# Optimization experiments

Hardware: AMD Instinct MI355X
Metric: run time of the kernel (lower is better)

## Reference

```python
import jax, jax.numpy as jnp
import numpy as np

BATCH, SEQ, N_INPUT, N_HIDDEN, N_OUTPUT = 256, 512, 512, 128, 2


def setup_inputs() -> dict:
    key = jax.random.key(0)
    ks = jax.random.split(key, 6)
    s_i = 1.0 / np.sqrt(N_INPUT)
    s_h = 1.0 / np.sqrt(N_HIDDEN)
    return {
        "x": jax.random.normal(ks[0], (BATCH, SEQ, N_INPUT), dtype=jnp.float32),
        # LSTM gate kernels, gate order (i, f, g, o) concatenated on last axis.
        # flax nn.LSTMCell: dense_i has no bias, dense_h has bias.
        "Wi": jax.random.normal(ks[1], (N_INPUT, 4 * N_HIDDEN), dtype=jnp.float32) * s_i,
        "Wh": jax.random.normal(ks[2], (N_HIDDEN, 4 * N_HIDDEN), dtype=jnp.float32) * s_h,
        "b": jax.random.normal(ks[3], (4 * N_HIDDEN,), dtype=jnp.float32) * 0.01,
        "Wd": jax.random.normal(ks[4], (N_HIDDEN, N_OUTPUT), dtype=jnp.float32) * s_h,
        "bd": jax.random.normal(ks[5], (N_OUTPUT,), dtype=jnp.float32) * 0.01,
    }


def reference(x, Wi, Wh, b, Wd, bd):
    B, S, _ = x.shape
    H = Wh.shape[0]
    # Precompute input projection for all steps in one big GEMM: (S, B, 4H)
    x_gates = jnp.einsum('bsi,ig->sbg', x, Wi)

    def step(carry, xg):
        c, h = carry
        gates = xg + h @ Wh + b  # (B, 4H)
        i, f, g, o = jnp.split(gates, 4, axis=-1)
        c = jax.nn.sigmoid(f) * c + jax.nn.sigmoid(i) * jnp.tanh(g)
        h = jax.nn.sigmoid(o) * jnp.tanh(c)
        return (c, h), h

    c0 = jnp.zeros((B, H), dtype=x.dtype)
    h0 = jnp.zeros((B, H), dtype=x.dtype)
    (_, h_last), _ = jax.lax.scan(step, (c0, h0), x_gates)
    logits = h_last @ Wd + bd  # (B, N_OUTPUT)
    return logits
```

## Files before the change

kernel.cpp:

```cpp
#include <hip/hip_runtime.h>
#include <hip/hip_bf16.h>


typedef __attribute__((ext_vector_type(8))) short short8;
typedef __attribute__((ext_vector_type(4))) float floatx4;
typedef __attribute__((ext_vector_type(4))) unsigned short ushortx4;
typedef __attribute__((ext_vector_type(2))) unsigned int uint2v;

#define LOG2E 1.44269504088896340736f

__device__ __forceinline__ unsigned short f2bf(float f) {
  unsigned int u = __builtin_bit_cast(unsigned int, f);
  u = (u + 0x7fffu + ((u >> 16) & 1u)) >> 16;
  return (unsigned short)u;
}
__device__ __forceinline__ float bf2f(unsigned short u) {
  unsigned int v = ((unsigned int)u) << 16;
  return __builtin_bit_cast(float, v);
}
__device__ __forceinline__ float sigf(float x) {
  return __builtin_amdgcn_rcpf(1.0f + __builtin_amdgcn_exp2f(-LOG2E * x));
}
__device__ __forceinline__ float tanhf_(float x) {
  return 1.0f - 2.0f * __builtin_amdgcn_rcpf(1.0f + __builtin_amdgcn_exp2f(2.0f * LOG2E * x));
}
__device__ __forceinline__ void bar_lds() {
  asm volatile("s_waitcnt lgkmcnt(0)" ::: "memory");
  __builtin_amdgcn_s_barrier();
  __builtin_amdgcn_sched_barrier(0);
}
__device__ __forceinline__ void gl_lds16(const void* g, void* l) {
  __builtin_amdgcn_global_load_lds(
      (const __attribute__((address_space(1))) unsigned int*)g,
      (__attribute__((address_space(3))) unsigned int*)l, 16, 0, 0);
}

__global__ void pack_kernel(const float* __restrict__ Wi, const float* __restrict__ Wh,
                            unsigned short* __restrict__ Wi_p, unsigned short* __restrict__ Wh_p,
                            unsigned int* __restrict__ flags) {
  if (blockIdx.x == 0 && threadIdx.x < 8) flags[threadIdx.x] = 0u;
  int idx = blockIdx.x * 256 + threadIdx.x;
  if (idx < 262144) {
    int j = idx & 7, lane = (idx >> 3) & 63, nt = (idx >> 9) & 31, kk = idx >> 14;
    int k = kk * 32 + ((lane >> 4) * 8) + j;
    int n = nt * 16 + (lane & 15);
    Wi_p[idx] = f2bf(Wi[k * 512 + n]);
  } else {
    int i2 = idx - 262144;
    int j = i2 & 7, lane = (i2 >> 3) & 63, nt = (i2 >> 9) & 31, kk = i2 >> 14;
    int k = kk * 32 + ((lane >> 4) * 8) + j;
    int n = nt * 16 + (lane & 15);
    Wh_p[i2] = f2bf(Wh[k * 512 + n]);
  }
}

__global__ __launch_bounds__(512, 2) void fused_kernel(
    const float* __restrict__ x, const unsigned short* __restrict__ Wi_p,
    const float* __restrict__ bias, unsigned int* __restrict__ xg5,
    const unsigned short* __restrict__ Wh_p, const float* __restrict__ Wd,
    const float* __restrict__ bd, float* __restrict__ out,
    unsigned int* __restrict__ flags) {
  __shared__ __align__(16) unsigned short As[128 * 72];
  __shared__ __align__(16) unsigned short Bs[2 * 32 * 64 * 8];
  __shared__ __align__(16) unsigned short hb[2 * 16 * 140];
  __shared__ __align__(16) float gbw[8 * 320];

  const int tid = threadIdx.x;
  const int lane = tid & 63;
  const int w = tid >> 6;
  const int quad = lane >> 4;
  const int lm = lane & 15;

  if (blockIdx.x < 192) {
    const int wm = w >> 2, wn = w & 3;

    float bs_[4][2];
    #pragma unroll
    for (int g = 0; g < 4; ++g)
      #pragma unroll
      for (int jc = 0; jc < 2; ++jc)
        bs_[g][jc] = bias[g * 128 + wn * 32 + jc * 16 + lm];

    for (int t = blockIdx.x; t < 1024; t += 192) {
      const int s = t >> 1;
      const int b0 = (t & 1) * 128;

      floatx4 acc[4][8];
      #pragma unroll
      for (int a = 0; a < 4; ++a)
        #pragma unroll
        for (int b2 = 0; b2 < 8; ++b2) { acc[a][b2].x = 0.f; acc[a][b2].y = 0.f; acc[a][b2].z = 0.f; acc[a][b2].w = 0.f; }

      const float* xbase = x + ((size_t)(b0 + w * 16 + quad) * 512 + s) * 512 + lm * 4;

      floatx4 cur[4], nxt[4];
      #pragma unroll
      for (int i = 0; i < 4; ++i)
        cur[i] = *(const floatx4*)(xbase + (size_t)i * 1048576);

      for (int kt = 0; kt < 8; ++kt) {
        bar_lds();
        #pragma unroll
        for (int i = 0; i < 4; ++i) {
          int r = w * 16 + i * 4 + quad;
          ushortx4 u;
          u.x = f2bf(cur[i].x); u.y = f2bf(cur[i].y); u.z = f2bf(cur[i].z); u.w = f2bf(cur[i].w);
          *(ushortx4*)(&As[r * 72 + lm * 4]) = u;
        }
        #pragma unroll
        for (int c = 0; c < 8; ++c) {
          int kg = c & 1, ntl = (c >> 1) * 8 + w;
          const unsigned short* src = Wi_p + ((size_t)((kt * 2 + kg) * 32 + ntl) * 64 + lane) * 8;
          unsigned short* dst = &Bs[(size_t)((kg * 32 + ntl) * 64) * 8];
          gl_lds16(src, dst);
        }
        __builtin_amdgcn_sched_barrier(0);
        if (kt < 7) {
          #pragma unroll
          for (int i = 0; i < 4; ++i)
            nxt[i] = *(const floatx4*)(xbase + (size_t)i * 1048576 + (kt + 1) * 64);
          asm volatile("s_waitcnt vmcnt(4) lgkmcnt(0)" ::: "memory");
        } else {
          asm volatile("s_waitcnt vmcnt(0) lgkmcnt(0)" ::: "memory");
        }
        __builtin_amdgcn_s_barrier();
        __builtin_amdgcn_sched_barrier(0);
        #pragma unroll
        for (int ks = 0; ks < 2; ++ks) {
          short8 af[4];
          #pragma unroll
          for (int mt = 0; mt < 4; ++mt) {
            int m = wm * 64 + mt * 16 + lm;
            af[mt] = *(const short8*)(&As[m * 72 + ks * 32 + quad * 8]);
          }
          #pragma unroll
          for (int nt = 0; nt < 8; ++nt) {
            int g = nt >> 1, jc = nt & 1;
            int ntl = g * 8 + wn * 2 + jc;
            short8 bfv = *(const short8*)(&Bs[(size_t)((ks * 32 + ntl) * 64 + lane) * 8]);
            #pragma unroll
            for (int mt = 0; mt < 4; ++mt)
              acc[mt][nt] = __builtin_amdgcn_mfma_f32_16x16x32_bf16(af[mt], bfv, acc[mt][nt], 0, 0, 0);
          }
        }
        #pragma unroll
        for (int i = 0; i < 4; ++i) cur[i] = nxt[i];
      }
      #pragma unroll
      for (int mt = 0; mt < 4; ++mt) {
        int bbase = b0 + wm * 64 + mt * 16 + quad * 4;
        #pragma unroll
        for (int jc = 0; jc < 2; ++jc) {
          int wv = wn * 2 + jc;
          #pragma unroll
          for (int rr = 0; rr < 4; ++rr) {
            size_t cell = ((size_t)s * 64 + ((bbase + rr) >> 2)) * 512 + wv * 64 + rr * 16 + lm;
            float g0 = acc[mt][0 + jc][rr] + bs_[0][jc];
            float g1 = acc[mt][2 + jc][rr] + bs_[1][jc];
            float g2 = acc[mt][4 + jc][rr] + bs_[2][jc];
            float g3 = acc[mt][6 + jc][rr] + bs_[3][jc];
            uint2v v;
            v.x = (unsigned int)f2bf(g0) | ((unsigned int)f2bf(g1) << 16);
            v.y = (unsigned int)f2bf(g2) | ((unsigned int)f2bf(g3) << 16);
            *(uint2v*)(xg5 + cell * 2) = v;
          }
        }
      }
      __syncthreads();
      if (tid == 0)
        __hip_atomic_fetch_add(&flags[t >> 7], 1u, __ATOMIC_RELEASE, __HIP_MEMORY_SCOPE_AGENT);
    }
  } else {
    const int bb = blockIdx.x - 192;

    for (int i = tid; i < 2 * 16 * 140; i += 512) hb[i] = 0;

    short8 bfr[4][4];
    #pragma unroll
    for (int kk = 0; kk < 4; ++kk)
      #pragma unroll
      for (int g = 0; g < 4; ++g)
        bfr[kk][g] = *(const short8*)(Wh_p + ((size_t)(kk * 32 + g * 8 + w) * 64 + lane) * 8);

    float cst = 0.f;

    const unsigned int* xp = xg5 + ((size_t)bb * 512 + tid) * 2;
    float* gw = gbw + w * 320;

    while (__hip_atomic_load(&flags[0], __ATOMIC_ACQUIRE, __HIP_MEMORY_SCOPE_AGENT) < 128u)
      __builtin_amdgcn_s_sleep(2);

    uint2v xga = *(const uint2v*)(xp);
    uint2v xgb = *(const uint2v*)(xp + 65536);

    __syncthreads();

    auto substep = [&](const int rp, uint2v& xcur, int spre) {
      uint2v xv = xcur;
      if (spre < 512)
        xcur = *(const uint2v*)(xp + (size_t)spre * 65536);

      short8 af[4];
      #pragma unroll
      for (int kk = 0; kk < 4; ++kk) {
        const unsigned short* p = &hb[rp * 2240 + lm * 140 + kk * 32 + quad * 8];
        union { short8 v; ushortx4 h[2]; } t;
        t.h[0] = *(const ushortx4*)(p);
        t.h[1] = *(const ushortx4*)(p + 4);
        af[kk] = t.v;
      }
      floatx4 acc[4];
      #pragma unroll
      for (int g = 0; g < 4; ++g) { acc[g].x = 0.f; acc[g].y = 0.f; acc[g].z = 0.f; acc[g].w = 0.f; }
      #pragma unroll
      for (int kk = 0; kk < 4; ++kk)
        #pragma unroll
        for (int g = 0; g < 4; ++g)
          acc[g] = __builtin_amdgcn_mfma_f32_16x16x32_bf16(af[kk], bfr[kk][g], acc[g], 0, 0, 0);

      if (lane < 16) {
        #pragma unroll
        for (int r = 0; r < 4; ++r) {
          floatx4 t4;
          t4.x = acc[0][r]; t4.y = acc[1][r]; t4.z = acc[2][r]; t4.w = acc[3][r];
          *(floatx4*)(gw + lm * 20 + r * 4) = t4;
        }
      }
      asm volatile("s_waitcnt lgkmcnt(0)" ::: "memory");
      __builtin_amdgcn_sched_barrier(0);
      floatx4 gv = *(const floatx4*)(gw + lm * 20 + quad * 4);

      float pre0 = gv.x + bf2f((unsigned short)(xv.x & 0xffffu));
      float pre1 = gv.y + bf2f((unsigned short)(xv.x >> 16));
      float pre2 = gv.z + bf2f((unsigned short)(xv.y & 0xffffu));
      float pre3 = gv.w + bf2f((unsigned short)(xv.y >> 16));
      float cc = sigf(pre1) * cst + sigf(pre0) * tanhf_(pre2);
      cst = cc;
      float hv = sigf(pre3) * tanhf_(cc);
      hb[(rp ^ 1) * 2240 + quad * 140 + w * 16 + lm] = f2bf(hv);
      bar_lds();
    };

    for (int c = 0; c < 8; ++c) {
      if (c < 7) {
        while (__hip_atomic_load(&flags[c + 1], __ATOMIC_ACQUIRE, __HIP_MEMORY_SCOPE_AGENT) < 128u)
          __builtin_amdgcn_s_sleep(2);
      }
      #pragma unroll 1
      for (int s2 = 0; s2 < 64; s2 += 2) {
        int s = c * 64 + s2;
        substep(0, xga, s + 2);
        substep(1, xgb, s + 3);
      }
    }

    if (tid < 8) {
      int rw = tid >> 1, co = tid & 1;
      float a = bd[co];
      for (int j2 = 0; j2 < 128; ++j2)
        a += bf2f(hb[rw * 140 + j2]) * Wd[j2 * 2 + co];
      out[(bb * 4 + rw) * 2 + co] = a;
    }
  }
}

extern "C" void kernel_launch(void* const* d_in, const int* in_sizes, int n_in,
                              void* d_out, int out_size, void* d_ws, size_t ws_size,
                              hipStream_t stream) {
  const float* x  = (const float*)d_in[0];
  const float* Wi = (const float*)d_in[1];
  const float* Wh = (const float*)d_in[2];
  const float* b  = (const float*)d_in[3];
  const float* Wd = (const float*)d_in[4];
  const float* bd = (const float*)d_in[5];
  float* out = (float*)d_out;

  unsigned short* Wi_p = (unsigned short*)d_ws;
  unsigned short* Wh_p = Wi_p + 262144;
  unsigned int*   flags = (unsigned int*)(Wh_p + 65536);
  unsigned int*   xg5  = flags + 128;

  pack_kernel<<<1280, 256, 0, stream>>>(Wi, Wh, Wi_p, Wh_p, flags);
  fused_kernel<<<256, 512, 0, stream>>>(x, Wi_p, b, xg5, Wh_p, Wd, bd, out, flags);
}
```

Baseline: 798.8 us.

## Use relaxed atomic xgate transfers and single-wave chunk flag polling

The producer blocks now write the bf16 gate pre-activations with 64-bit relaxed agent-scope atomic stores. The recurrent blocks read them with matching atomic loads. Only wave 0 of each recurrent block spins on the chunk flag, and it polls the current chunk rather than the next one; the other waves then pass an LDS barrier and reload the first two steps' inputs at each chunk start. This is meant to cut polling traffic and keep cross-block data coherent, but it drops the one-chunk lookahead and uses relaxed ordering in place of acquire, so the consumer may stall at chunk boundaries and could read stale data.

```diff
diff --git a/kernel.cpp b/kernel.cpp
--- a/kernel.cpp
+++ b/kernel.cpp
@@ -159,14 +159,16 @@
             float g1 = acc[mt][2 + jc][rr] + bs_[1][jc];
             float g2 = acc[mt][4 + jc][rr] + bs_[2][jc];
             float g3 = acc[mt][6 + jc][rr] + bs_[3][jc];
-            uint2v v;
-            v.x = (unsigned int)f2bf(g0) | ((unsigned int)f2bf(g1) << 16);
-            v.y = (unsigned int)f2bf(g2) | ((unsigned int)f2bf(g3) << 16);
-            *(uint2v*)(xg5 + cell * 2) = v;
+            unsigned long long v64 =
+                (unsigned long long)((unsigned int)f2bf(g0) | ((unsigned int)f2bf(g1) << 16)) |
+                ((unsigned long long)((unsigned int)f2bf(g2) | ((unsigned int)f2bf(g3) << 16)) << 32);
+            __hip_atomic_store((unsigned long long*)xg5 + cell, v64,
+                               __ATOMIC_RELAXED, __HIP_MEMORY_SCOPE_AGENT);
           }
         }
       }
       __syncthreads();
+      __builtin_amdgcn_sched_barrier(0);
       if (tid == 0)
         __hip_atomic_fetch_add(&flags[t >> 7], 1u, __ATOMIC_RELEASE, __HIP_MEMORY_SCOPE_AGENT);
     }
@@ -184,21 +186,22 @@
 
     float cst = 0.f;
 
-    const unsigned int* xp = xg5 + ((size_t)bb * 512 + tid) * 2;
+    const unsigned long long* xp = (const unsigned long long*)xg5 + ((size_t)bb * 512 + tid);
     float* gw = gbw + w * 320;
 
-    while (__hip_atomic_load(&flags[0], __ATOMIC_ACQUIRE, __HIP_MEMORY_SCOPE_AGENT) < 128u)
-      __builtin_amdgcn_s_sleep(2);
-
-    uint2v xga = *(const uint2v*)(xp);
-    uint2v xgb = *(const uint2v*)(xp + 65536);
+    auto at_load8 = [](const unsigned long long* p) -> uint2v {
+      unsigned long long v = __hip_atomic_load(p, __ATOMIC_RELAXED, __HIP_MEMORY_SCOPE_AGENT);
+      uint2v r; r.x = (unsigned int)v; r.y = (unsigned int)(v >> 32); return r;
+    };
 
     __syncthreads();
+
+    uint2v xga, xgb;
 
     auto substep = [&](const int rp, uint2v& xcur, int spre) {
       uint2v xv = xcur;
       if (spre < 512)
-        xcur = *(const uint2v*)(xp + (size_t)spre * 65536);
+        xcur = at_load8(xp + (size_t)spre * 32768);
 
       short8 af[4];
       #pragma unroll
@@ -242,10 +245,13 @@
     };
 
     for (int c = 0; c < 8; ++c) {
-      if (c < 7) {
-        while (__hip_atomic_load(&flags[c + 1], __ATOMIC_ACQUIRE, __HIP_MEMORY_SCOPE_AGENT) < 128u)
+      if (w == 0) {
+        while (__hip_atomic_load(&flags[c], __ATOMIC_RELAXED, __HIP_MEMORY_SCOPE_AGENT) < 128u)
           __builtin_amdgcn_s_sleep(2);
       }
+      bar_lds();
+      xga = at_load8(xp + (size_t)(c * 64) * 32768);
+      xgb = at_load8(xp + (size_t)(c * 64 + 1) * 32768);
       #pragma unroll 1
       for (int s2 = 0; s2 < 64; s2 += 2) {
         int s = c * 64 + s2;
```

After: 686.4 us. -14.1%, faster.
